# Kernel optimization log

Hardware: AMD Instinct MI355X
Metric: run time of the kernel (lower is better)

Reference implementation:

```python
import jax, jax.numpy as jnp
import numpy as np
from math import sqrt

D = 512        # output_dim (layer_dims[-1])
H = 4          # num_heads
ATN = D // H   # atn_dim = 128
BERT_D = 768
B = 32         # number of graph pairs
NP = 4096
NH = 4096


def setup_inputs() -> dict:
    key = jax.random.key(0)
    ks = jax.random.split(key, 20)
    inp = {
        'ctx_p': jax.random.normal(ks[0], (NP, D), jnp.float32),
        'ctx_h': jax.random.normal(ks[1], (NH, D), jnp.float32),
        'lhs_p': jax.random.normal(ks[2], (NP, BERT_D), jnp.float32),
        'lhs_h': jax.random.normal(ks[3], (NH, BERT_D), jnp.float32),
        'batch_p': jnp.sort(jax.random.randint(ks[4], (NP,), 0, B)).astype(jnp.int64),
        'batch_h': jnp.sort(jax.random.randint(ks[5], (NH,), 0, B)).astype(jnp.int64),
        # learned parameters (stored [in, out])
        'Wq': jax.random.normal(ks[6], (D, D), jnp.float32) * 0.02,
        'bq': jnp.zeros((D,), jnp.float32),
        'Wk': jax.random.normal(ks[7], (D, D), jnp.float32) * 0.02,
        'bk': jnp.zeros((D,), jnp.float32),
        'Wv': jax.random.normal(ks[8], (BERT_D, BERT_D), jnp.float32) * 0.02,
        'bv': jnp.zeros((BERT_D,), jnp.float32),
        'W1': jax.random.normal(ks[9], (D + BERT_D, 256), jnp.float32) * 0.02,
        'b1': jnp.zeros((256,), jnp.float32),
        'W2': jax.random.normal(ks[10], (256, 128), jnp.float32) * 0.02,
        'ln_g': jnp.ones((128,), jnp.float32),
        'ln_b': jnp.zeros((128,), jnp.float32),
        'Wc': jax.random.normal(ks[11], (128, 3), jnp.float32) * 0.02,
        'bc': jnp.zeros((3,), jnp.float32),
    }
    return inp


def reference(ctx_p, ctx_h, lhs_p, lhs_h, batch_p, batch_h,
              Wq, bq, Wk, bk, Wv, bv, W1, b1, W2, ln_g, ln_b, Wc, bc):
    # q/k projections; torch code does .view(-1, atn_dim, num_heads) -> head is fastest axis
    qs = (ctx_h @ Wq + bq).reshape(-1, ATN, H)          # [nh, atn, H]
    ks = (ctx_p @ Wk + bk).reshape(-1, ATN, H)          # [np, atn, H]
    vs = (lhs_p @ Wv + bv).reshape(-1, H, BERT_D // H)  # [np, H, 768/H]

    atn = jnp.einsum('ndh,mdh->nmh', qs, ks) / sqrt(ATN)  # [nh, np, H]
    # faithful to original: positions where batch ids MATCH are set to -1e10
    mask_same = batch_h[:, None] == batch_p[None, :]       # [nh, np]
    atn = jnp.where(mask_same[:, :, None], jnp.float32(-1e10), atn)
    atn = jax.nn.softmax(atn, axis=1)                      # softmax over premise words m

    attended = jnp.einsum('nmh,mhd->nhd', atn, vs).reshape(-1, BERT_D)  # [nh, 768]

    feats = jnp.concatenate([ctx_h, lhs_h - attended], axis=1)  # [nh, D+768]
    h1 = jax.nn.gelu(feats @ W1 + b1, approximate=False)
    h2 = h1 @ W2                                                # Linear no bias
    mu = h2.mean(axis=-1, keepdims=True)
    var = ((h2 - mu) ** 2).mean(axis=-1, keepdims=True)
    h2 = (h2 - mu) * jax.lax.rsqrt(var + 1e-5) * ln_g + ln_b    # LayerNorm(128)

    # global_mean_pool over batch_h
    pooled = jax.ops.segment_sum(h2, batch_h, num_segments=B)
    counts = jax.ops.segment_sum(jnp.ones((h2.shape[0], 1), h2.dtype), batch_h, num_segments=B)
    pooled = pooled / jnp.maximum(counts, 1.0)

    return pooled @ Wc + bc  # [B, 3]
```

## Files before the change

kernel.cpp:

```cpp
#include <hip/hip_runtime.h>
#include <hip/hip_bf16.h>
#include <math.h>

#define NP_N 4096
#define NH_N 4096
#define D_N 512
#define BERT_N 768
#define H_N 4
#define B_N 32
#define SCL2 0.12754245006257576f

typedef __attribute__((ext_vector_type(8))) short short8;
typedef __attribute__((ext_vector_type(4))) float f32x4;
typedef __attribute__((ext_vector_type(4))) unsigned short ush4;
typedef __attribute__((ext_vector_type(4))) unsigned int uivec4;
typedef unsigned short ushort_t;

__device__ __forceinline__ void gl_lds16(const void* g, void* l) {
    __builtin_amdgcn_global_load_lds((const __attribute__((address_space(1))) void*)g,
                                     (__attribute__((address_space(3))) void*)l, 16, 0, 0);
}
__device__ __forceinline__ unsigned short f2bu(float f) {
    __hip_bfloat16 b = __float2bfloat16(f);
    return *reinterpret_cast<unsigned short*>(&b);
}
__device__ __forceinline__ float b2f(unsigned short u) {
    union { unsigned int i; float f; } x; x.i = ((unsigned int)u) << 16; return x.f;
}
__device__ __forceinline__ unsigned int pkbf(float a, float b) {
    union { __hip_bfloat162 h; unsigned int u; } x;
    x.h.x = __float2bfloat16(a);
    x.h.y = __float2bfloat16(b);
    return x.u;
}
__device__ __forceinline__ unsigned int sxor(unsigned int v, int m) {
    return (unsigned int)__shfl_xor((int)v, m);
}

__device__ __forceinline__ short8 mkfrag(uint2 u, uint2 v, bool hi, bool godd) {
    unsigned ux32 = sxor(u.x, 32), uy32 = sxor(u.y, 32);
    unsigned vx32 = sxor(v.x, 32), vy32 = sxor(v.y, 32);
    unsigned ax = hi ? vx32 : u.x, bx = hi ? v.x : ux32;
    unsigned ay = hi ? vy32 : u.y, by = hi ? v.y : uy32;
    unsigned sbx = sxor(bx, 16), sax = sxor(ax, 16);
    unsigned sby = sxor(by, 16), say = sxor(ay, 16);
    uivec4 w;
    w.x = godd ? sbx : ax;
    w.y = godd ? sby : ay;
    w.z = godd ? bx : sax;
    w.w = godd ? by : say;
    return __builtin_bit_cast(short8, w);
}

#define EW_BLOCKS 512
__global__ __launch_bounds__(256) void convert_all(
    const float* __restrict__ ctx_h, const float* __restrict__ ctx_p,
    const float* __restrict__ lhs_p,
    const float* __restrict__ Wq, const float* __restrict__ Wk,
    const float* __restrict__ Wv, const float* __restrict__ W1,
    const float* __restrict__ bq, const float* __restrict__ bk,
    ushort_t* __restrict__ ctxp_bf, ushort_t* __restrict__ lhsp_bf,
    ushort_t* __restrict__ feats,
    ushort_t* __restrict__ Wqt, ushort_t* __restrict__ Wkt,
    ushort_t* __restrict__ Wvt, ushort_t* __restrict__ W1t,
    float* __restrict__ bqp, float* __restrict__ bkp)
{
    const int bid = blockIdx.x, t = threadIdx.x;
    if (bid < EW_BLOCKS) {
        const long N0 = 524288, N1 = 1048576, TOT = 1835008;
        for (long i = (long)bid * 256 + t; i < TOT; i += (long)EW_BLOCKS * 256) {
            float4 v; ush4 o;
            if (i < N0) {
                long k = i;
                v = ((const float4*)ctx_h)[k];
                o[0] = f2bu(v.x); o[1] = f2bu(v.y); o[2] = f2bu(v.z); o[3] = f2bu(v.w);
                long n = k >> 7, c4 = k & 127;
                ((ush4*)feats)[n * 320 + c4] = o;
            } else if (i < N1) {
                long k = i - N0;
                v = ((const float4*)ctx_p)[k];
                o[0] = f2bu(v.x); o[1] = f2bu(v.y); o[2] = f2bu(v.z); o[3] = f2bu(v.w);
                ((ush4*)ctxp_bf)[k] = o;
            } else {
                long k = i - N1;
                v = ((const float4*)lhs_p)[k];
                o[0] = f2bu(v.x); o[1] = f2bu(v.y); o[2] = f2bu(v.z); o[3] = f2bu(v.w);
                ((ush4*)lhsp_bf)[k] = o;
            }
        }
        if (bid == 0) {
            for (int n = t; n < 512; n += 256) {
                int np = (n & 3) * 128 + (n >> 2);
                bqp[np] = bq[n] * SCL2;
                bkp[np] = bk[n];
            }
        }
        return;
    }
    int tb = bid - EW_BLOCKS;
    const float* src; ushort_t* dst; int K, N, tile, perm; float wscl;
    if (tb < 64)       { src = Wq; dst = Wqt; K = 512;  N = 512; tile = tb;       perm = 1; wscl = SCL2; }
    else if (tb < 128) { src = Wk; dst = Wkt; K = 512;  N = 512; tile = tb - 64;  perm = 1; wscl = 1.f; }
    else if (tb < 272) { src = Wv; dst = Wvt; K = 768;  N = 768; tile = tb - 128; perm = 0; wscl = 1.f; }
    else               { src = W1; dst = W1t; K = 1280; N = 256; tile = tb - 272; perm = 0; wscl = 1.f; }
    int ntn = N >> 6;
    int k0 = (tile / ntn) * 64, n0 = (tile % ntn) * 64;
    __shared__ float tl[64][65];
#pragma unroll
    for (int i = 0; i < 16; i++) {
        int idx = t + i * 256; int r = idx >> 6, c = idx & 63;
        tl[r][c] = src[(size_t)(k0 + r) * N + n0 + c];
    }
    __syncthreads();
#pragma unroll
    for (int i = 0; i < 16; i++) {
        int idx = t + i * 256; int r = idx >> 6, c = idx & 63;
        int n = n0 + r;
        int nr = perm ? ((n & 3) * 128 + (n >> 2)) : n;
        dst[(size_t)nr * K + k0 + c] = f2bu(tl[c][r] * wscl);
    }
}

template<int TM, int TN, int BIAS_ROW, int GELU>
__global__ __launch_bounds__(256) void gemm2(
    const ushort_t* __restrict__ A, int lda, const ushort_t* __restrict__ Bt,
    const float* __restrict__ bias, ushort_t* __restrict__ C,
    int M, int N, int K)
{
    constexpr int MF = TM / 32, NF = TN / 32;
    constexpr int AI = TM / 32, BI = TN / 32;
    __shared__ ushort_t As[2][TM * 64];
    __shared__ ushort_t Bs[2][TN * 64];
    const int t = threadIdx.x, w = t >> 6, lane = t & 63;
    const int lq = lane & 15, g = lane >> 4;
    const int wm = w >> 1, wn = w & 1;
    const int n0 = blockIdx.x * TN, m0 = blockIdx.y * TM;
    const int nsteps = K >> 6;

    f32x4 acc[MF][NF] = {};

    auto STAGE = [&](int buf, int k0) {
#pragma unroll
        for (int jj = 0; jj < AI; jj++) {
            int j = w * AI + jj;
            int r = j * 8 + (lane >> 3);
            int c = (lane & 7) * 16;
            int cs = c ^ ((r & 7) << 4);
            gl_lds16((const char*)A + ((size_t)(m0 + r) * lda + k0) * 2 + cs,
                     (void*)&As[buf][j * 512]);
        }
#pragma unroll
        for (int jj = 0; jj < BI; jj++) {
            int j = w * BI + jj;
            int r = j * 8 + (lane >> 3);
            int c = (lane & 7) * 16;
            int cs = c ^ ((r & 7) << 4);
            gl_lds16((const char*)Bt + ((size_t)(n0 + r) * K + k0) * 2 + cs,
                     (void*)&Bs[buf][j * 512]);
        }
    };

    STAGE(0, 0);
    asm volatile("s_waitcnt vmcnt(0)" ::: "memory");
    __builtin_amdgcn_s_barrier();
    int cur = 0;
    for (int s = 0; s < nsteps; s++) {
        if (s + 1 < nsteps) STAGE(cur ^ 1, (s + 1) * 64);
        const char* Ab = (const char*)&As[cur][0];
        const char* Bb = (const char*)&Bs[cur][0];
        const int swz = (lq & 7) << 4;
        short8 af[MF][2], bfr[NF][2];
#pragma unroll
        for (int mf = 0; mf < MF; mf++) {
            int r = wm * (TM / 2) + mf * 16 + lq;
#pragma unroll
            for (int ks = 0; ks < 2; ks++)
                af[mf][ks] = *(const short8*)(Ab + r * 128 + ((ks * 64 + g * 16) ^ swz));
        }
#pragma unroll
        for (int nf = 0; nf < NF; nf++) {
            int r = wn * (TN / 2) + nf * 16 + lq;
#pragma unroll
            for (int ks = 0; ks < 2; ks++)
                bfr[nf][ks] = *(const short8*)(Bb + r * 128 + ((ks * 64 + g * 16) ^ swz));
        }
        __builtin_amdgcn_s_setprio(1);
#pragma unroll
        for (int mf = 0; mf < MF; mf++)
#pragma unroll
            for (int nf = 0; nf < NF; nf++)
#pragma unroll
                for (int ks = 0; ks < 2; ks++)
                    acc[mf][nf] = __builtin_amdgcn_mfma_f32_16x16x32_bf16(
                        af[mf][ks], bfr[nf][ks], acc[mf][nf], 0, 0, 0);
        __builtin_amdgcn_s_setprio(0);
        asm volatile("s_waitcnt vmcnt(0)" ::: "memory");
        __builtin_amdgcn_s_barrier();
        cur ^= 1;
    }

#pragma unroll
    for (int mf = 0; mf < MF; mf++) {
#pragma unroll
        for (int nf = 0; nf < NF; nf++) {
            int ncol = n0 + wn * (TN / 2) + nf * 16 + lq;
            float bcol = BIAS_ROW ? 0.f : bias[ncol];
#pragma unroll
            for (int j = 0; j < 4; j++) {
                int mrow = m0 + wm * (TM / 2) + mf * 16 + 4 * g + j;
                float v = acc[mf][nf][j] + (BIAS_ROW ? bias[mrow] : bcol);
                if (GELU) v = 0.5f * v * (1.f + erff(v * 0.70710678118654752f));
                C[(size_t)mrow * N + ncol] = f2bu(v);
            }
        }
    }
}

__global__ __launch_bounds__(512, 2) void attn_mfma(
    const ushort_t* __restrict__ Qb,
    const ushort_t* __restrict__ Kb,
    const ushort_t* __restrict__ Vtb,
    const int* __restrict__ batch_h, const int* __restrict__ batch_p,
    ushort_t* __restrict__ Opart,
    float* __restrict__ ml)
{
    const int bid = blockIdx.x;
    const int h = (bid & 7) >> 1;
    const int s = bid & 1;
    const int n0 = (bid >> 3) * 128;

    __shared__ __align__(16) char smem[163840];

    const int t = threadIdx.x;
    const int w = t >> 6, o = w >> 2, wq = w & 3;
    const int lane = t & 63, lq = lane & 15, g = lane >> 4;
    const int lqm = (lq & 7) << 4;
    const bool hi = lane >= 32;
    const bool godd = (lane & 16) != 0;

    char* Kt0 = smem + (o * 2 + 0) * 16384;
    char* Kt1 = smem + (o * 2 + 1) * 16384;
    char* Vt0 = smem + 65536 + (o * 2 + 0) * 24576;
    char* Vt1 = smem + 65536 + (o * 2 + 1) * 24576;

    short8 qf[2][4];
    int bhq[2];
#pragma unroll
    for (int qg = 0; qg < 2; qg++) {
        const ushort_t* qrow = Qb + (size_t)(n0 + wq * 32 + qg * 16 + lq) * 512 + h * 128;
#pragma unroll
        for (int ks = 0; ks < 4; ks++)
            qf[qg][ks] = *(const short8*)(qrow + ks * 32 + g * 8);
        bhq[qg] = batch_h[n0 + wq * 32 + qg * 16 + lq];
    }

    f32x4 Ofr[2][12];
#pragma unroll
    for (int qg = 0; qg < 2; qg++)
#pragma unroll
        for (int nt = 0; nt < 12; nt++) Ofr[qg][nt] = (f32x4){0.f, 0.f, 0.f, 0.f};
    float m_run[2] = {-1e30f, -1e30f}, l_run[2] = {0.f, 0.f};

    const char* Kg = (const char*)Kb;
    const char* Vg = (const char*)Vtb;
    const int kb = s * 2048 + o * 1024;

    auto STAGE = [&](char* Kd, char* Vd, int m0k) {
#pragma unroll
        for (int jj = 0; jj < 4; jj++) {
            int j = wq * 4 + jj;
            int r = j * 4 + (lane >> 4);
            int c = (lane & 15) * 16;
            gl_lds16(Kg + (size_t)(m0k + r) * 1024 + h * 256 + (c ^ ((r & 7) << 4)),
                     Kd + j * 1024);
        }
#pragma unroll
        for (int jj = 0; jj < 6; jj++) {
            int j = wq * 6 + jj;
            int r = j * 8 + (lane >> 3);
            int c = (lane & 7) * 16;
            gl_lds16(Vg + ((size_t)(h * 192 + r) * 4096 + m0k) * 2 + (c ^ ((r & 7) << 4)),
                     Vd + j * 1024);
        }
    };

    STAGE(Kt0, Vt0, kb);
    asm volatile("s_waitcnt vmcnt(0)" ::: "memory");
    __builtin_amdgcn_s_barrier();
    int cur = 0;

    for (int tile = 0; tile < 16; tile++) {
        char* Kc = cur ? Kt1 : Kt0;
        char* Vc = cur ? Vt1 : Vt0;
        const int ktb = kb + tile * 64;

        int4 bp4[4];
#pragma unroll
        for (int mt = 0; mt < 4; mt++)
            bp4[mt] = *(const int4*)&batch_p[ktb + mt * 16 + 4 * g];

        if (tile + 1 < 16) STAGE(cur ? Kt0 : Kt1, cur ? Vt0 : Vt1, kb + (tile + 1) * 64);

        f32x4 S[2][4];
#pragma unroll
        for (int qg = 0; qg < 2; qg++)
#pragma unroll
            for (int mt = 0; mt < 4; mt++) S[qg][mt] = (f32x4){0.f, 0.f, 0.f, 0.f};
        __builtin_amdgcn_s_setprio(1);
#pragma unroll
        for (int mt = 0; mt < 4; mt++) {
            const char* rbase = Kc + (mt * 16 + lq) * 256;
#pragma unroll
            for (int ks = 0; ks < 4; ks++) {
                short8 kf = *(const short8*)(rbase + ((ks * 64 + g * 16) ^ lqm));
                S[0][mt] = __builtin_amdgcn_mfma_f32_16x16x32_bf16(kf, qf[0][ks], S[0][mt], 0, 0, 0);
                S[1][mt] = __builtin_amdgcn_mfma_f32_16x16x32_bf16(kf, qf[1][ks], S[1][mt], 0, 0, 0);
            }
        }
        __builtin_amdgcn_s_setprio(0);

        float pmax[2];
#pragma unroll
        for (int qg = 0; qg < 2; qg++) {
            float m = -1e30f;
#pragma unroll
            for (int mt = 0; mt < 4; mt++) {
                float v0 = (bp4[mt].x == bhq[qg]) ? -1e9f : S[qg][mt][0];
                float v1 = (bp4[mt].y == bhq[qg]) ? -1e9f : S[qg][mt][1];
                float v2 = (bp4[mt].z == bhq[qg]) ? -1e9f : S[qg][mt][2];
                float v3 = (bp4[mt].w == bhq[qg]) ? -1e9f : S[qg][mt][3];
                S[qg][mt][0] = v0; S[qg][mt][1] = v1; S[qg][mt][2] = v2; S[qg][mt][3] = v3;
                m = fmaxf(m, fmaxf(fmaxf(v0, v1), fmaxf(v2, v3)));
            }
            pmax[qg] = m;
        }
        bool ng = __all((pmax[0] <= m_run[0] + 8.f) && (pmax[1] <= m_run[1] + 8.f));
        if (!ng) {
#pragma unroll
            for (int qg = 0; qg < 2; qg++) {
                float mq = fmaxf(pmax[qg], m_run[qg]);
                mq = fmaxf(mq, __shfl_xor(mq, 16));
                mq = fmaxf(mq, __shfl_xor(mq, 32));
                float f = exp2f(m_run[qg] - mq);
                m_run[qg] = mq;
                l_run[qg] *= f;
                float fr0 = __shfl(f, 4 * g + 0);
                float fr1 = __shfl(f, 4 * g + 1);
                float fr2 = __shfl(f, 4 * g + 2);
                float fr3 = __shfl(f, 4 * g + 3);
#pragma unroll
                for (int nt = 0; nt < 12; nt++) {
                    Ofr[qg][nt][0] *= fr0; Ofr[qg][nt][1] *= fr1;
                    Ofr[qg][nt][2] *= fr2; Ofr[qg][nt][3] *= fr3;
                }
            }
        }

        uint2 P2[2][4];
#pragma unroll
        for (int qg = 0; qg < 2; qg++) {
            float lsum = 0.f;
#pragma unroll
            for (int mt = 0; mt < 4; mt++) {
                float e0 = exp2f(S[qg][mt][0] - m_run[qg]);
                float e1 = exp2f(S[qg][mt][1] - m_run[qg]);
                float e2 = exp2f(S[qg][mt][2] - m_run[qg]);
                float e3 = exp2f(S[qg][mt][3] - m_run[qg]);
                lsum += (e0 + e1) + (e2 + e3);
                P2[qg][mt].x = pkbf(e0, e1);
                P2[qg][mt].y = pkbf(e2, e3);
            }
            l_run[qg] += lsum;
        }

#pragma unroll
        for (int ks = 0; ks < 2; ks++) {
            short8 pf0 = mkfrag(P2[0][2 * ks], P2[0][2 * ks + 1], hi, godd);
            short8 pf1 = mkfrag(P2[1][2 * ks], P2[1][2 * ks + 1], hi, godd);
            __builtin_amdgcn_s_setprio(1);
#pragma unroll
            for (int nt = 0; nt < 12; nt++) {
                short8 vf = *(const short8*)(Vc + (nt * 16 + lq) * 128 + ((ks * 64 + g * 16) ^ lqm));
                Ofr[0][nt] = __builtin_amdgcn_mfma_f32_16x16x32_bf16(pf0, vf, Ofr[0][nt], 0, 0, 0);
                Ofr[1][nt] = __builtin_amdgcn_mfma_f32_16x16x32_bf16(pf1, vf, Ofr[1][nt], 0, 0, 0);
            }
            __builtin_amdgcn_s_setprio(0);
        }

        asm volatile("s_waitcnt vmcnt(0)" ::: "memory");
        __builtin_amdgcn_s_barrier();
        cur ^= 1;
    }

    float lt[2];
#pragma unroll
    for (int qg = 0; qg < 2; qg++) {
        float l = l_run[qg];
        l += __shfl_xor(l, 16);
        l += __shfl_xor(l, 32);
        lt[qg] = l;
    }

    const int tq = wq * 64 + lane;
    float* mOf = (float*)smem;
    float* mls = (float*)(smem + 98304);
    if (o == 1) {
#pragma unroll
        for (int qg = 0; qg < 2; qg++) {
#pragma unroll
            for (int nt = 0; nt < 12; nt++)
                *(f32x4*)(mOf + tq * 96 + qg * 48 + nt * 4) = Ofr[qg][nt];
            if (g == 0) {
                mls[(wq * 16 + lq) * 4 + qg * 2 + 0] = m_run[qg];
                mls[(wq * 16 + lq) * 4 + qg * 2 + 1] = lt[qg];
            }
        }
    }
    __syncthreads();
    if (o == 0) {
        const size_t plane = (size_t)(s * 4 + h) * 4096;
#pragma unroll
        for (int qg = 0; qg < 2; qg++) {
            float m1 = mls[(wq * 16 + lq) * 4 + qg * 2 + 0];
            float l1 = mls[(wq * 16 + lq) * 4 + qg * 2 + 1];
            float m = fmaxf(m_run[qg], m1);
            float a0 = exp2f(m_run[qg] - m), a1 = exp2f(m1 - m);
            float l = lt[qg] * a0 + l1 * a1;
            int qrow = n0 + wq * 32 + qg * 16;
            if (g == 0) {
                ml[(plane + qrow + lq) * 2 + 0] = m;
                ml[(plane + qrow + lq) * 2 + 1] = l;
            }
            float f0[4], f1[4];
#pragma unroll
            for (int j = 0; j < 4; j++) {
                f0[j] = __shfl(a0, 4 * g + j);
                f1[j] = __shfl(a1, 4 * g + j);
            }
#pragma unroll
            for (int nt = 0; nt < 12; nt++) {
                f32x4 o1 = *(f32x4*)(mOf + tq * 96 + qg * 48 + nt * 4);
#pragma unroll
                for (int j = 0; j < 4; j++) {
                    float val = Ofr[qg][nt][j] * f0[j] + o1[j] * f1[j];
                    Opart[(plane + qrow + 4 * g + j) * 192 + nt * 16 + lq] = f2bu(val);
                }
            }
        }
    }
}

__global__ __launch_bounds__(256) void combine_feats(
    const ushort_t* __restrict__ Opart, const float* __restrict__ ml,
    const float* __restrict__ lhs_h, ushort_t* __restrict__ feats)
{
    const int t = threadIdx.x;
#pragma unroll
    for (int i = 0; i < 4; i++) {
        int q = blockIdx.x * 4 + i;
#pragma unroll
        for (int it = 0; it < 3; it++) {
            int c = t + it * 256;
            int h = c / 192, vd = c - h * 192;
            size_t i0 = (size_t)h * 4096 + q;
            size_t i1 = (size_t)(4 + h) * 4096 + q;
            float m0 = ml[i0 * 2], l0 = ml[i0 * 2 + 1];
            float m1 = ml[i1 * 2], l1 = ml[i1 * 2 + 1];
            float m = fmaxf(m0, m1);
            float e0 = exp2f(m0 - m), e1 = exp2f(m1 - m);
            float linv = 1.f / (l0 * e0 + l1 * e1);
            float O = (b2f(Opart[i0 * 192 + vd]) * e0 + b2f(Opart[i1 * 192 + vd]) * e1) * linv;
            feats[(size_t)q * 1280 + 512 + c] = f2bu(lhs_h[(size_t)q * 768 + c] - O);
        }
    }
}

__global__ __launch_bounds__(256) void h2_ln(
    const ushort_t* __restrict__ h1, const float* __restrict__ W2,
    const float* __restrict__ ln_g, const float* __restrict__ ln_b,
    float* __restrict__ h2out)
{
    const int n0 = blockIdx.x * 8;
    const int t = threadIdx.x;
    __shared__ float h1s[8][256];
    __shared__ float h2s[8][128];

#pragma unroll
    for (int i = 0; i < 8; i++) {
        int idx = t + i * 256; int r = idx >> 8, c = idx & 255;
        h1s[r][c] = b2f(h1[(size_t)(n0 + r) * 256 + c]);
    }
    __syncthreads();

    {
        int o2 = t & 127, gq = t >> 7;
        float acc[4] = {};
        for (int k4 = 0; k4 < 64; k4++) {
            float w0 = W2[(size_t)(k4 * 4 + 0) * 128 + o2];
            float w1 = W2[(size_t)(k4 * 4 + 1) * 128 + o2];
            float w2 = W2[(size_t)(k4 * 4 + 2) * 128 + o2];
            float w3 = W2[(size_t)(k4 * 4 + 3) * 128 + o2];
#pragma unroll
            for (int q = 0; q < 4; q++) {
                float4 hh = *(const float4*)&h1s[gq * 4 + q][k4 * 4];
                acc[q] += hh.x * w0 + hh.y * w1 + hh.z * w2 + hh.w * w3;
            }
        }
#pragma unroll
        for (int q = 0; q < 4; q++) h2s[gq * 4 + q][o2] = acc[q];
    }
    __syncthreads();

    {
        int wv = t >> 6, lane = t & 63;
#pragma unroll
        for (int sx = 0; sx < 2; sx++) {
            int nd = wv * 2 + sx;
            float x0 = h2s[nd][lane], x1 = h2s[nd][lane + 64];
            float sum = x0 + x1;
#pragma unroll
            for (int off = 32; off; off >>= 1) sum += __shfl_xor(sum, off);
            float mu = sum * (1.f / 128.f);
            float d0 = x0 - mu, d1 = x1 - mu;
            float s2 = d0 * d0 + d1 * d1;
#pragma unroll
            for (int off = 32; off; off >>= 1) s2 += __shfl_xor(s2, off);
            float rstd = rsqrtf(s2 * (1.f / 128.f) + 1e-5f);
            size_t base = (size_t)(n0 + nd) * 128;
            h2out[base + lane]      = d0 * rstd * ln_g[lane] + ln_b[lane];
            h2out[base + lane + 64] = d1 * rstd * ln_g[lane + 64] + ln_b[lane + 64];
        }
    }
}

__global__ void ranges_kernel(const int* __restrict__ bh, int* __restrict__ lo,
                              int Nn, int Bn)
{
    int n = blockIdx.x * blockDim.x + threadIdx.x;
    if (n >= Nn) return;
    int b = bh[n];
    int prev = (n == 0) ? -1 : bh[n - 1];
    for (int bb = prev + 1; bb <= b; bb++) lo[bb] = n;
    if (n == Nn - 1) for (int bb = b + 1; bb <= Bn; bb++) lo[bb] = Nn;
}

__global__ __launch_bounds__(128) void pool_cls(
    const float* __restrict__ h2, const int* __restrict__ lo,
    const float* __restrict__ Wc, const float* __restrict__ bc,
    float* __restrict__ out)
{
    int b = blockIdx.x, t = threadIdx.x;
    int s = lo[b], e = lo[b + 1];
    float acc = 0.f;
    for (int n = s; n < e; n++) acc += h2[(size_t)n * 128 + t];
    float pooled = acc / fmaxf((float)(e - s), 1.f);
    __shared__ float red[128];
    for (int c = 0; c < 3; c++) {
        red[t] = pooled * Wc[t * 3 + c];
        __syncthreads();
        for (int off = 64; off > 0; off >>= 1) {
            if (t < off) red[t] += red[t + off];
            __syncthreads();
        }
        if (t == 0) out[b * 3 + c] = red[0] + bc[c];
        __syncthreads();
    }
}

extern "C" void kernel_launch(void* const* d_in, const int* in_sizes, int n_in,
                              void* d_out, int out_size, void* d_ws, size_t ws_size,
                              hipStream_t stream)
{
    const float* ctx_p  = (const float*)d_in[0];
    const float* ctx_h  = (const float*)d_in[1];
    const float* lhs_p  = (const float*)d_in[2];
    const float* lhs_h  = (const float*)d_in[3];
    const int*   batch_p = (const int*)d_in[4];
    const int*   batch_h = (const int*)d_in[5];
    const float* Wq = (const float*)d_in[6];
    const float* bq = (const float*)d_in[7];
    const float* Wk = (const float*)d_in[8];
    const float* bk = (const float*)d_in[9];
    const float* Wv = (const float*)d_in[10];
    const float* bv = (const float*)d_in[11];
    const float* W1 = (const float*)d_in[12];
    const float* b1 = (const float*)d_in[13];
    const float* W2 = (const float*)d_in[14];
    const float* ln_g = (const float*)d_in[15];
    const float* ln_b = (const float*)d_in[16];
    const float* Wc = (const float*)d_in[17];
    const float* bc = (const float*)d_in[18];
    float* out = (float*)d_out;

    ushort_t* u = (ushort_t*)d_ws;
    ushort_t* ctxp_bf = u;
    ushort_t* lhsp_bf = ctxp_bf + 2097152;
    ushort_t* Wqt  = lhsp_bf + 3145728;
    ushort_t* Wkt  = Wqt + 262144;
    ushort_t* Wvt  = Wkt + 262144;
    ushort_t* Opart = u;
    ushort_t* W1t  = Wvt + 589824;
    ushort_t* Qb   = W1t + 327680;
    ushort_t* Kb   = Qb + 2097152;
    ushort_t* Vtb  = Kb + 2097152;
    ushort_t* feats = Vtb + 3145728;
    ushort_t* h1   = feats + 5242880;
    float* ml  = (float*)(h1 + 1048576);
    float* h2  = ml + 65536;
    float* bqp = h2 + 524288;
    float* bkp = bqp + 512;
    int*   lo  = (int*)(bkp + 512);

    convert_all<<<864, 256, 0, stream>>>(
        ctx_h, ctx_p, lhs_p, Wq, Wk, Wv, W1, bq, bk,
        ctxp_bf, lhsp_bf, feats, Wqt, Wkt, Wvt, W1t, bqp, bkp);

    gemm2<128, 64, 0, 0><<<dim3(8, 32), 256, 0, stream>>>(feats, 1280, Wqt, bqp, Qb, NH_N, 512, 512);
    gemm2<128, 64, 0, 0><<<dim3(8, 32), 256, 0, stream>>>(ctxp_bf, 512, Wkt, bkp, Kb, NP_N, 512, 512);
    gemm2<128, 64, 1, 0><<<dim3(64, 6), 256, 0, stream>>>(Wvt, 768, lhsp_bf, bv, Vtb, 768, NP_N, 768);

    attn_mfma<<<256, 512, 0, stream>>>(Qb, Kb, Vtb, batch_h, batch_p, Opart, ml);

    combine_feats<<<1024, 256, 0, stream>>>(Opart, ml, lhs_h, feats);

    gemm2<64, 64, 0, 1><<<dim3(4, 64), 256, 0, stream>>>(feats, 1280, W1t, b1, h1, NH_N, 256, 1280);

    h2_ln<<<512, 256, 0, stream>>>(h1, W2, ln_g, ln_b, h2);
    ranges_kernel<<<16, 256, 0, stream>>>(batch_h, lo, NH_N, B_N);
    pool_cls<<<B_N, 128, 0, stream>>>(h2, lo, Wc, bc, out);
}
```

Before: 202.8 us.

## Merge QKV GEMMs, skip fully-masked attention tiles, drop ranges kernel

```diff
diff --git a/kernel.cpp b/kernel.cpp
--- a/kernel.cpp
+++ b/kernel.cpp
@@ -121,14 +121,126 @@
     }
 }
 
-template<int TM, int TN, int BIAS_ROW, int GELU>
-__global__ __launch_bounds__(256) void gemm2(
+__global__ __launch_bounds__(256) void gemm_qkv(
+    const ushort_t* __restrict__ feats, const ushort_t* __restrict__ ctxp,
+    const ushort_t* __restrict__ Wqt, const ushort_t* __restrict__ Wkt,
+    const ushort_t* __restrict__ Wvt, const ushort_t* __restrict__ lhsp,
+    const float* __restrict__ bqp, const float* __restrict__ bkp,
+    const float* __restrict__ bv,
+    ushort_t* __restrict__ Qb, ushort_t* __restrict__ Kb,
+    ushort_t* __restrict__ Vtb)
+{
+    int b = blockIdx.x;
+    const ushort_t *A, *Bt; const float* bias; ushort_t* C;
+    int lda, N, K, m0, n0, bias_row;
+    if (b < 256) {
+        A = feats; lda = 1280; Bt = Wqt; bias = bqp; C = Qb;
+        N = 512; K = 512; bias_row = 0;
+        n0 = (b & 7) * 64; m0 = (b >> 3) * 128;
+    } else if (b < 512) {
+        b -= 256;
+        A = ctxp; lda = 512; Bt = Wkt; bias = bkp; C = Kb;
+        N = 512; K = 512; bias_row = 0;
+        n0 = (b & 7) * 64; m0 = (b >> 3) * 128;
+    } else {
+        b -= 512;
+        A = Wvt; lda = 768; Bt = lhsp; bias = bv; C = Vtb;
+        N = 4096; K = 768; bias_row = 1;
+        n0 = (b & 63) * 64; m0 = (b >> 6) * 128;
+    }
+    const int nsteps = K >> 6;
+
+    __shared__ ushort_t As[2][128 * 64];
+    __shared__ ushort_t Bs[2][64 * 64];
+    const int t = threadIdx.x, w = t >> 6, lane = t & 63;
+    const int lq = lane & 15, g = lane >> 4;
+    const int wm = w >> 1, wn = w & 1;
+
+    f32x4 acc[4][2] = {};
+
+    auto STAGE = [&](int buf, int k0) {
+#pragma unroll
+        for (int jj = 0; jj < 4; jj++) {
+            int j = w * 4 + jj;
+            int r = j * 8 + (lane >> 3);
+            int c = (lane & 7) * 16;
+            int cs = c ^ ((r & 7) << 4);
+            gl_lds16((const char*)A + ((size_t)(m0 + r) * lda + k0) * 2 + cs,
+                     (void*)&As[buf][j * 512]);
+        }
+#pragma unroll
+        for (int jj = 0; jj < 2; jj++) {
+            int j = w * 2 + jj;
+            int r = j * 8 + (lane >> 3);
+            int c = (lane & 7) * 16;
+            int cs = c ^ ((r & 7) << 4);
+            gl_lds16((const char*)Bt + ((size_t)(n0 + r) * K + k0) * 2 + cs,
+                     (void*)&Bs[buf][j * 512]);
+        }
+    };
+
+    STAGE(0, 0);
+    asm volatile("s_waitcnt vmcnt(0)" ::: "memory");
+    __builtin_amdgcn_s_barrier();
+    int cur = 0;
+    for (int s = 0; s < nsteps; s++) {
+        if (s + 1 < nsteps) STAGE(cur ^ 1, (s + 1) * 64);
+        const char* Ab = (const char*)&As[cur][0];
+        const char* Bb = (const char*)&Bs[cur][0];
+        const int swz = (lq & 7) << 4;
+        short8 af[4][2], bfr[2][2];
+#pragma unroll
+        for (int mf = 0; mf < 4; mf++) {
+            int r = wm * 64 + mf * 16 + lq;
+#pragma unroll
+            for (int ks = 0; ks < 2; ks++)
+                af[mf][ks] = *(const short8*)(Ab + r * 128 + ((ks * 64 + g * 16) ^ swz));
+        }
+#pragma unroll
+        for (int nf = 0; nf < 2; nf++) {
+            int r = wn * 32 + nf * 16 + lq;
+#pragma unroll
+            for (int ks = 0; ks < 2; ks++)
+                bfr[nf][ks] = *(const short8*)(Bb + r * 128 + ((ks * 64 + g * 16) ^ swz));
+        }
+        __builtin_amdgcn_s_setprio(1);
+#pragma unroll
+        for (int mf = 0; mf < 4; mf++)
+#pragma unroll
+            for (int nf = 0; nf < 2; nf++)
+#pragma unroll
+                for (int ks = 0; ks < 2; ks++)
+                    acc[mf][nf] = __builtin_amdgcn_mfma_f32_16x16x32_bf16(
+                        af[mf][ks], bfr[nf][ks], acc[mf][nf], 0, 0, 0);
+        __builtin_amdgcn_s_setprio(0);
+        asm volatile("s_waitcnt vmcnt(0)" ::: "memory");
+        __builtin_amdgcn_s_barrier();
+        cur ^= 1;
+    }
+
+#pragma unroll
+    for (int mf = 0; mf < 4; mf++) {
+#pragma unroll
+        for (int nf = 0; nf < 2; nf++) {
+            int ncol = n0 + wn * 32 + nf * 16 + lq;
+            float bcol = bias_row ? 0.f : bias[ncol];
+#pragma unroll
+            for (int j = 0; j < 4; j++) {
+                int mrow = m0 + wm * 64 + mf * 16 + 4 * g + j;
+                float v = acc[mf][nf][j] + (bias_row ? bias[mrow] : bcol);
+                C[(size_t)mrow * N + ncol] = f2bu(v);
+            }
+        }
+    }
+}
+
+template<int TM, int TN>
+__global__ __launch_bounds__(256) void gemm_mlp1(
     const ushort_t* __restrict__ A, int lda, const ushort_t* __restrict__ Bt,
     const float* __restrict__ bias, ushort_t* __restrict__ C,
     int M, int N, int K)
 {
     constexpr int MF = TM / 32, NF = TN / 32;
-    constexpr int AI = TM / 32, BI = TN / 32;
     __shared__ ushort_t As[2][TM * 64];
     __shared__ ushort_t Bs[2][TN * 64];
     const int t = threadIdx.x, w = t >> 6, lane = t & 63;
@@ -141,8 +253,8 @@
 
     auto STAGE = [&](int buf, int k0) {
 #pragma unroll
-        for (int jj = 0; jj < AI; jj++) {
-            int j = w * AI + jj;
+        for (int jj = 0; jj < TM / 32; jj++) {
+            int j = w * (TM / 32) + jj;
             int r = j * 8 + (lane >> 3);
             int c = (lane & 7) * 16;
             int cs = c ^ ((r & 7) << 4);
@@ -150,8 +262,8 @@
                      (void*)&As[buf][j * 512]);
         }
 #pragma unroll
-        for (int jj = 0; jj < BI; jj++) {
-            int j = w * BI + jj;
+        for (int jj = 0; jj < TN / 32; jj++) {
+            int j = w * (TN / 32) + jj;
             int r = j * 8 + (lane >> 3);
             int c = (lane & 7) * 16;
             int cs = c ^ ((r & 7) << 4);
@@ -204,19 +316,19 @@
 #pragma unroll
         for (int nf = 0; nf < NF; nf++) {
             int ncol = n0 + wn * (TN / 2) + nf * 16 + lq;
-            float bcol = BIAS_ROW ? 0.f : bias[ncol];
+            float bcol = bias[ncol];
 #pragma unroll
             for (int j = 0; j < 4; j++) {
                 int mrow = m0 + wm * (TM / 2) + mf * 16 + 4 * g + j;
-                float v = acc[mf][nf][j] + (BIAS_ROW ? bias[mrow] : bcol);
-                if (GELU) v = 0.5f * v * (1.f + erff(v * 0.70710678118654752f));
+                float v = acc[mf][nf][j] + bcol;
+                v = 0.5f * v * (1.f + erff(v * 0.70710678118654752f));
                 C[(size_t)mrow * N + ncol] = f2bu(v);
             }
         }
     }
 }
 
-__global__ __launch_bounds__(512, 2) void attn_mfma(
+__global__ __launch_bounds__(512, 4) void attn_mfma(
     const ushort_t* __restrict__ Qb,
     const ushort_t* __restrict__ Kb,
     const ushort_t* __restrict__ Vtb,
@@ -229,54 +341,58 @@
     const int s = bid & 1;
     const int n0 = (bid >> 3) * 128;
 
-    __shared__ __align__(16) char smem[163840];
+    __shared__ __align__(16) char smem[81920];
 
     const int t = threadIdx.x;
-    const int w = t >> 6, o = w >> 2, wq = w & 3;
+    const int w = t >> 6;
     const int lane = t & 63, lq = lane & 15, g = lane >> 4;
     const int lqm = (lq & 7) << 4;
     const bool hi = lane >= 32;
     const bool godd = (lane & 16) != 0;
 
-    char* Kt0 = smem + (o * 2 + 0) * 16384;
-    char* Kt1 = smem + (o * 2 + 1) * 16384;
-    char* Vt0 = smem + 65536 + (o * 2 + 0) * 24576;
-    char* Vt1 = smem + 65536 + (o * 2 + 1) * 24576;
-
-    short8 qf[2][4];
-    int bhq[2];
-#pragma unroll
-    for (int qg = 0; qg < 2; qg++) {
-        const ushort_t* qrow = Qb + (size_t)(n0 + wq * 32 + qg * 16 + lq) * 512 + h * 128;
+    char* Kt0 = smem;
+    char* Kt1 = smem + 16384;
+    char* Vt0 = smem + 32768;
+    char* Vt1 = smem + 32768 + 24576;
+
+    short8 qf[4];
+    {
+        const ushort_t* qrow = Qb + (size_t)(n0 + w * 16 + lq) * 512 + h * 128;
 #pragma unroll
         for (int ks = 0; ks < 4; ks++)
-            qf[qg][ks] = *(const short8*)(qrow + ks * 32 + g * 8);
-        bhq[qg] = batch_h[n0 + wq * 32 + qg * 16 + lq];
-    }
-
-    f32x4 Ofr[2][12];
-#pragma unroll
-    for (int qg = 0; qg < 2; qg++)
-#pragma unroll
-        for (int nt = 0; nt < 12; nt++) Ofr[qg][nt] = (f32x4){0.f, 0.f, 0.f, 0.f};
-    float m_run[2] = {-1e30f, -1e30f}, l_run[2] = {0.f, 0.f};
+            qf[ks] = *(const short8*)(qrow + ks * 32 + g * 8);
+    }
+    const int bhq = batch_h[n0 + w * 16 + lq];
+    const int bh_lo = batch_h[n0 + w * 16];
+    const int bh_hi = batch_h[n0 + w * 16 + 15];
+
+    f32x4 Ofr[12];
+#pragma unroll
+    for (int nt = 0; nt < 12; nt++) Ofr[nt] = (f32x4){0.f, 0.f, 0.f, 0.f};
+    float m_run = -1e30f, l_run = 0.f;
 
     const char* Kg = (const char*)Kb;
     const char* Vg = (const char*)Vtb;
-    const int kb = s * 2048 + o * 1024;
+    const int kb = s * 2048;
+
+    int tlo = 0, thi = 0;
+    if (lane < 32) {
+        tlo = batch_p[kb + lane * 64];
+        thi = batch_p[kb + lane * 64 + 63];
+    }
 
     auto STAGE = [&](char* Kd, char* Vd, int m0k) {
 #pragma unroll
-        for (int jj = 0; jj < 4; jj++) {
-            int j = wq * 4 + jj;
+        for (int jj = 0; jj < 2; jj++) {
+            int j = w * 2 + jj;
             int r = j * 4 + (lane >> 4);
             int c = (lane & 15) * 16;
             gl_lds16(Kg + (size_t)(m0k + r) * 1024 + h * 256 + (c ^ ((r & 7) << 4)),
                      Kd + j * 1024);
         }
 #pragma unroll
-        for (int jj = 0; jj < 6; jj++) {
-            int j = wq * 6 + jj;
+        for (int jj = 0; jj < 3; jj++) {
+            int j = w * 3 + jj;
             int r = j * 8 + (lane >> 3);
             int c = (lane & 7) * 16;
             gl_lds16(Vg + ((size_t)(h * 192 + r) * 4096 + m0k) * 2 + (c ^ ((r & 7) << 4)),
@@ -289,102 +405,95 @@
     __builtin_amdgcn_s_barrier();
     int cur = 0;
 
-    for (int tile = 0; tile < 16; tile++) {
+    for (int tile = 0; tile < 32; tile++) {
         char* Kc = cur ? Kt1 : Kt0;
         char* Vc = cur ? Vt1 : Vt0;
         const int ktb = kb + tile * 64;
-
-        int4 bp4[4];
-#pragma unroll
-        for (int mt = 0; mt < 4; mt++)
-            bp4[mt] = *(const int4*)&batch_p[ktb + mt * 16 + 4 * g];
-
-        if (tile + 1 < 16) STAGE(cur ? Kt0 : Kt1, cur ? Vt0 : Vt1, kb + (tile + 1) * 64);
-
-        f32x4 S[2][4];
-#pragma unroll
-        for (int qg = 0; qg < 2; qg++)
-#pragma unroll
-            for (int mt = 0; mt < 4; mt++) S[qg][mt] = (f32x4){0.f, 0.f, 0.f, 0.f};
-        __builtin_amdgcn_s_setprio(1);
-#pragma unroll
-        for (int mt = 0; mt < 4; mt++) {
-            const char* rbase = Kc + (mt * 16 + lq) * 256;
-#pragma unroll
-            for (int ks = 0; ks < 4; ks++) {
-                short8 kf = *(const short8*)(rbase + ((ks * 64 + g * 16) ^ lqm));
-                S[0][mt] = __builtin_amdgcn_mfma_f32_16x16x32_bf16(kf, qf[0][ks], S[0][mt], 0, 0, 0);
-                S[1][mt] = __builtin_amdgcn_mfma_f32_16x16x32_bf16(kf, qf[1][ks], S[1][mt], 0, 0, 0);
-            }
-        }
-        __builtin_amdgcn_s_setprio(0);
-
-        float pmax[2];
-#pragma unroll
-        for (int qg = 0; qg < 2; qg++) {
-            float m = -1e30f;
+        const int klo = __shfl(tlo, tile);
+        const int khi = __shfl(thi, tile);
+        const bool allmask = (klo == khi) && (klo == bh_lo) && (bh_lo == bh_hi);
+        const bool needmask = (klo <= bh_hi) && (khi >= bh_lo);
+
+        if (tile + 1 < 32) STAGE(cur ? Kt0 : Kt1, cur ? Vt0 : Vt1, kb + (tile + 1) * 64);
+
+        if (!allmask) {
+            f32x4 S[4];
+#pragma unroll
+            for (int mt = 0; mt < 4; mt++) S[mt] = (f32x4){0.f, 0.f, 0.f, 0.f};
+            __builtin_amdgcn_s_setprio(1);
 #pragma unroll
             for (int mt = 0; mt < 4; mt++) {
-                float v0 = (bp4[mt].x == bhq[qg]) ? -1e9f : S[qg][mt][0];
-                float v1 = (bp4[mt].y == bhq[qg]) ? -1e9f : S[qg][mt][1];
-                float v2 = (bp4[mt].z == bhq[qg]) ? -1e9f : S[qg][mt][2];
-                float v3 = (bp4[mt].w == bhq[qg]) ? -1e9f : S[qg][mt][3];
-                S[qg][mt][0] = v0; S[qg][mt][1] = v1; S[qg][mt][2] = v2; S[qg][mt][3] = v3;
-                m = fmaxf(m, fmaxf(fmaxf(v0, v1), fmaxf(v2, v3)));
-            }
-            pmax[qg] = m;
-        }
-        bool ng = __all((pmax[0] <= m_run[0] + 8.f) && (pmax[1] <= m_run[1] + 8.f));
-        if (!ng) {
-#pragma unroll
-            for (int qg = 0; qg < 2; qg++) {
-                float mq = fmaxf(pmax[qg], m_run[qg]);
+                const char* rbase = Kc + (mt * 16 + lq) * 256;
+#pragma unroll
+                for (int ks = 0; ks < 4; ks++) {
+                    short8 kf = *(const short8*)(rbase + ((ks * 64 + g * 16) ^ lqm));
+                    S[mt] = __builtin_amdgcn_mfma_f32_16x16x32_bf16(kf, qf[ks], S[mt], 0, 0, 0);
+                }
+            }
+            __builtin_amdgcn_s_setprio(0);
+
+            float pmax = -1e30f;
+            if (needmask) {
+#pragma unroll
+                for (int mt = 0; mt < 4; mt++) {
+                    int4 bp = *(const int4*)&batch_p[ktb + mt * 16 + 4 * g];
+                    float v0 = (bp.x == bhq) ? -1e9f : S[mt][0];
+                    float v1 = (bp.y == bhq) ? -1e9f : S[mt][1];
+                    float v2 = (bp.z == bhq) ? -1e9f : S[mt][2];
+                    float v3 = (bp.w == bhq) ? -1e9f : S[mt][3];
+                    S[mt][0] = v0; S[mt][1] = v1; S[mt][2] = v2; S[mt][3] = v3;
+                    pmax = fmaxf(pmax, fmaxf(fmaxf(v0, v1), fmaxf(v2, v3)));
+                }
+            } else {
+#pragma unroll
+                for (int mt = 0; mt < 4; mt++)
+                    pmax = fmaxf(pmax, fmaxf(fmaxf(S[mt][0], S[mt][1]),
+                                             fmaxf(S[mt][2], S[mt][3])));
+            }
+            bool ng = __all(pmax <= m_run + 8.f);
+            if (!ng) {
+                float mq = fmaxf(pmax, m_run);
                 mq = fmaxf(mq, __shfl_xor(mq, 16));
                 mq = fmaxf(mq, __shfl_xor(mq, 32));
-                float f = exp2f(m_run[qg] - mq);
-                m_run[qg] = mq;
-                l_run[qg] *= f;
+                float f = exp2f(m_run - mq);
+                m_run = mq;
+                l_run *= f;
                 float fr0 = __shfl(f, 4 * g + 0);
                 float fr1 = __shfl(f, 4 * g + 1);
                 float fr2 = __shfl(f, 4 * g + 2);
                 float fr3 = __shfl(f, 4 * g + 3);
 #pragma unroll
                 for (int nt = 0; nt < 12; nt++) {
-                    Ofr[qg][nt][0] *= fr0; Ofr[qg][nt][1] *= fr1;
-                    Ofr[qg][nt][2] *= fr2; Ofr[qg][nt][3] *= fr3;
+                    Ofr[nt][0] *= fr0; Ofr[nt][1] *= fr1;
+                    Ofr[nt][2] *= fr2; Ofr[nt][3] *= fr3;
                 }
             }
-        }
-
-        uint2 P2[2][4];
-#pragma unroll
-        for (int qg = 0; qg < 2; qg++) {
+
+            uint2 P2[4];
             float lsum = 0.f;
 #pragma unroll
             for (int mt = 0; mt < 4; mt++) {
-                float e0 = exp2f(S[qg][mt][0] - m_run[qg]);
-                float e1 = exp2f(S[qg][mt][1] - m_run[qg]);
-                float e2 = exp2f(S[qg][mt][2] - m_run[qg]);
-                float e3 = exp2f(S[qg][mt][3] - m_run[qg]);
+                float e0 = exp2f(S[mt][0] - m_run);
+                float e1 = exp2f(S[mt][1] - m_run);
+                float e2 = exp2f(S[mt][2] - m_run);
+                float e3 = exp2f(S[mt][3] - m_run);
                 lsum += (e0 + e1) + (e2 + e3);
-                P2[qg][mt].x = pkbf(e0, e1);
-                P2[qg][mt].y = pkbf(e2, e3);
-            }
-            l_run[qg] += lsum;
-        }
-
-#pragma unroll
-        for (int ks = 0; ks < 2; ks++) {
-            short8 pf0 = mkfrag(P2[0][2 * ks], P2[0][2 * ks + 1], hi, godd);
-            short8 pf1 = mkfrag(P2[1][2 * ks], P2[1][2 * ks + 1], hi, godd);
-            __builtin_amdgcn_s_setprio(1);
-#pragma unroll
-            for (int nt = 0; nt < 12; nt++) {
-                short8 vf = *(const short8*)(Vc + (nt * 16 + lq) * 128 + ((ks * 64 + g * 16) ^ lqm));
-                Ofr[0][nt] = __builtin_amdgcn_mfma_f32_16x16x32_bf16(pf0, vf, Ofr[0][nt], 0, 0, 0);
-                Ofr[1][nt] = __builtin_amdgcn_mfma_f32_16x16x32_bf16(pf1, vf, Ofr[1][nt], 0, 0, 0);
-            }
-            __builtin_amdgcn_s_setprio(0);
+                P2[mt].x = pkbf(e0, e1);
+                P2[mt].y = pkbf(e2, e3);
+            }
+            l_run += lsum;
+
+#pragma unroll
+            for (int ks = 0; ks < 2; ks++) {
+                short8 pf = mkfrag(P2[2 * ks], P2[2 * ks + 1], hi, godd);
+                __builtin_amdgcn_s_setprio(1);
+#pragma unroll
+                for (int nt = 0; nt < 12; nt++) {
+                    short8 vf = *(const short8*)(Vc + (nt * 16 + lq) * 128 + ((ks * 64 + g * 16) ^ lqm));
+                    Ofr[nt] = __builtin_amdgcn_mfma_f32_16x16x32_bf16(pf, vf, Ofr[nt], 0, 0, 0);
+                }
+                __builtin_amdgcn_s_setprio(0);
+            }
         }
 
         asm volatile("s_waitcnt vmcnt(0)" ::: "memory");
@@ -392,61 +501,21 @@
         cur ^= 1;
     }
 
-    float lt[2];
-#pragma unroll
-    for (int qg = 0; qg < 2; qg++) {
-        float l = l_run[qg];
-        l += __shfl_xor(l, 16);
-        l += __shfl_xor(l, 32);
-        lt[qg] = l;
-    }
-
-    const int tq = wq * 64 + lane;
-    float* mOf = (float*)smem;
-    float* mls = (float*)(smem + 98304);
-    if (o == 1) {
-#pragma unroll
-        for (int qg = 0; qg < 2; qg++) {
-#pragma unroll
-            for (int nt = 0; nt < 12; nt++)
-                *(f32x4*)(mOf + tq * 96 + qg * 48 + nt * 4) = Ofr[qg][nt];
-            if (g == 0) {
-                mls[(wq * 16 + lq) * 4 + qg * 2 + 0] = m_run[qg];
-                mls[(wq * 16 + lq) * 4 + qg * 2 + 1] = lt[qg];
-            }
-        }
-    }
-    __syncthreads();
-    if (o == 0) {
-        const size_t plane = (size_t)(s * 4 + h) * 4096;
-#pragma unroll
-        for (int qg = 0; qg < 2; qg++) {
-            float m1 = mls[(wq * 16 + lq) * 4 + qg * 2 + 0];
-            float l1 = mls[(wq * 16 + lq) * 4 + qg * 2 + 1];
-            float m = fmaxf(m_run[qg], m1);
-            float a0 = exp2f(m_run[qg] - m), a1 = exp2f(m1 - m);
-            float l = lt[qg] * a0 + l1 * a1;
-            int qrow = n0 + wq * 32 + qg * 16;
-            if (g == 0) {
-                ml[(plane + qrow + lq) * 2 + 0] = m;
-                ml[(plane + qrow + lq) * 2 + 1] = l;
-            }
-            float f0[4], f1[4];
-#pragma unroll
-            for (int j = 0; j < 4; j++) {
-                f0[j] = __shfl(a0, 4 * g + j);
-                f1[j] = __shfl(a1, 4 * g + j);
-            }
-#pragma unroll
-            for (int nt = 0; nt < 12; nt++) {
-                f32x4 o1 = *(f32x4*)(mOf + tq * 96 + qg * 48 + nt * 4);
-#pragma unroll
-                for (int j = 0; j < 4; j++) {
-                    float val = Ofr[qg][nt][j] * f0[j] + o1[j] * f1[j];
-                    Opart[(plane + qrow + 4 * g + j) * 192 + nt * 16 + lq] = f2bu(val);
-                }
-            }
-        }
+    float l = l_run;
+    l += __shfl_xor(l, 16);
+    l += __shfl_xor(l, 32);
+
+    const size_t plane = (size_t)(s * 4 + h) * 4096;
+    const int q0 = n0 + w * 16;
+    if (g == 0) {
+        ml[(plane + q0 + lq) * 2 + 0] = m_run;
+        ml[(plane + q0 + lq) * 2 + 1] = l;
+    }
+#pragma unroll
+    for (int nt = 0; nt < 12; nt++) {
+#pragma unroll
+        for (int j = 0; j < 4; j++)
+            Opart[(plane + q0 + 4 * g + j) * 192 + nt * 16 + lq] = f2bu(Ofr[nt][j]);
     }
 }
 
@@ -533,24 +602,24 @@
     }
 }
 
-__global__ void ranges_kernel(const int* __restrict__ bh, int* __restrict__ lo,
-                              int Nn, int Bn)
-{
-    int n = blockIdx.x * blockDim.x + threadIdx.x;
-    if (n >= Nn) return;
-    int b = bh[n];
-    int prev = (n == 0) ? -1 : bh[n - 1];
-    for (int bb = prev + 1; bb <= b; bb++) lo[bb] = n;
-    if (n == Nn - 1) for (int bb = b + 1; bb <= Bn; bb++) lo[bb] = Nn;
-}
-
 __global__ __launch_bounds__(128) void pool_cls(
-    const float* __restrict__ h2, const int* __restrict__ lo,
+    const float* __restrict__ h2, const int* __restrict__ batch_h,
     const float* __restrict__ Wc, const float* __restrict__ bc,
     float* __restrict__ out)
 {
     int b = blockIdx.x, t = threadIdx.x;
-    int s = lo[b], e = lo[b + 1];
+    __shared__ int bounds[2];
+    if (t < 2) {
+        int target = b + t;
+        int lo = 0, hi = NH_N;
+        while (lo < hi) {
+            int mid = (lo + hi) >> 1;
+            if (batch_h[mid] < target) lo = mid + 1; else hi = mid;
+        }
+        bounds[t] = lo;
+    }
+    __syncthreads();
+    int s = bounds[0], e = bounds[1];
     float acc = 0.f;
     for (int n = s; n < e; n++) acc += h2[(size_t)n * 128 + t];
     float pooled = acc / fmaxf((float)(e - s), 1.f);
@@ -609,23 +678,20 @@
     float* h2  = ml + 65536;
     float* bqp = h2 + 524288;
     float* bkp = bqp + 512;
-    int*   lo  = (int*)(bkp + 512);
 
     convert_all<<<864, 256, 0, stream>>>(
         ctx_h, ctx_p, lhs_p, Wq, Wk, Wv, W1, bq, bk,
         ctxp_bf, lhsp_bf, feats, Wqt, Wkt, Wvt, W1t, bqp, bkp);
 
-    gemm2<128, 64, 0, 0><<<dim3(8, 32), 256, 0, stream>>>(feats, 1280, Wqt, bqp, Qb, NH_N, 512, 512);
-    gemm2<128, 64, 0, 0><<<dim3(8, 32), 256, 0, stream>>>(ctxp_bf, 512, Wkt, bkp, Kb, NP_N, 512, 512);
-    gemm2<128, 64, 1, 0><<<dim3(64, 6), 256, 0, stream>>>(Wvt, 768, lhsp_bf, bv, Vtb, 768, NP_N, 768);
+    gemm_qkv<<<896, 256, 0, stream>>>(
+        feats, ctxp_bf, Wqt, Wkt, Wvt, lhsp_bf, bqp, bkp, bv, Qb, Kb, Vtb);
 
     attn_mfma<<<256, 512, 0, stream>>>(Qb, Kb, Vtb, batch_h, batch_p, Opart, ml);
 
     combine_feats<<<1024, 256, 0, stream>>>(Opart, ml, lhs_h, feats);
 
-    gemm2<64, 64, 0, 1><<<dim3(4, 64), 256, 0, stream>>>(feats, 1280, W1t, b1, h1, NH_N, 256, 1280);
+    gemm_mlp1<64, 64><<<dim3(4, 64), 256, 0, stream>>>(feats, 1280, W1t, b1, h1, NH_N, 256, 1280);
 
     h2_ln<<<512, 256, 0, stream>>>(h1, W2, ln_g, ln_b, h2);
-    ranges_kernel<<<16, 256, 0, stream>>>(batch_h, lo, NH_N, B_N);
-    pool_cls<<<B_N, 128, 0, stream>>>(h2, lo, Wc, bc, out);
-}
+    pool_cls<<<B_N, 128, 0, stream>>>(h2, batch_h, Wc, bc, out);
+}
```

New measurement: 221.1 us. 1.09x slower.
